# Kernel optimization log

Measured on AMD Instinct MI355X. Metric: run time of the kernel, lower is better.

The kernel has to match this reference:

```python
import jax, jax.numpy as jnp
import numpy as np

N_NODES = 50000
N_EDGES = 600000
D = 128
APPNP_K = 5
APPNP_ALPHA = 0.2


def _mish(x):
    return x * jnp.tanh(jax.nn.softplus(x))


def setup_inputs() -> dict:
    key = jax.random.key(0)
    ks = jax.random.split(key, 6)
    x = jax.random.normal(ks[0], (N_NODES, D), dtype=jnp.float32)
    src = jax.random.randint(ks[1], (N_EDGES,), 0, N_NODES, dtype=jnp.int32)
    dst = jax.random.randint(ks[2], (N_EDGES,), 0, N_NODES, dtype=jnp.int32)
    W1 = jax.random.normal(ks[3], (D, D), dtype=jnp.float32) * (1.0 / np.sqrt(D))
    b1 = jnp.zeros((D,), dtype=jnp.float32)
    W2 = jax.random.normal(ks[4], (2 * D, D), dtype=jnp.float32) * (1.0 / np.sqrt(2 * D))
    b2 = jnp.zeros((D,), dtype=jnp.float32)
    eps1 = jnp.zeros((1,), dtype=jnp.float32)
    eps2 = jnp.zeros((1,), dtype=jnp.float32)
    return {"x": x, "src": src, "dst": dst, "W1": W1, "b1": b1,
            "W2": W2, "b2": b2, "eps1": eps1, "eps2": eps2}


def _appnp(x0, src, dst):
    # DGL APPNPConv: symmetric degree normalization, k power-iteration steps.
    ones = jnp.ones((src.shape[0],), dtype=x0.dtype)
    deg_out = jnp.clip(jax.ops.segment_sum(ones, src, num_segments=N_NODES), 1.0)
    deg_in = jnp.clip(jax.ops.segment_sum(ones, dst, num_segments=N_NODES), 1.0)
    norm_o = deg_out[:, None] ** -0.5  # [N,1]
    norm_i = deg_in[:, None] ** -0.5
    h = x0
    for _ in range(APPNP_K):
        h = h * norm_o
        h = jax.ops.segment_sum(h[src], dst, num_segments=N_NODES)  # gather-scatter
        h = h * norm_i
        h = (1.0 - APPNP_ALPHA) * h + APPNP_ALPHA * x0
    return h


def _gin(h, src, dst, eps, W, b):
    # GINConv(sum, learn_eps): (1+eps)*h + sum_{j in N(i)} h_j, then Linear.
    agg = jax.ops.segment_sum(h[src], dst, num_segments=N_NODES)
    return ((1.0 + eps) * h + agg) @ W + b


def reference(x, src, dst, W1, b1, W2, b2, eps1, eps2):
    out = jnp.tanh(x)           # GCNNorm affects edge weights only; node feats then tanh
    x0 = out                    # res_out[0]
    out = _appnp(out, src, dst)
    out = _gin(out, src, dst, eps1[0], W1, b1)          # layer 0
    out = jnp.concatenate([out, x0], axis=1)            # residual concat
    out = _gin(out, src, dst, eps2[0], W2, b2)          # layer 1
    return _mish(out)
```

## Files before the change

### kernel.cpp

```cpp
#include <hip/hip_runtime.h>
#include <hip/hip_fp16.h>
#include <math.h>

#define NN 50000
#define NE 600000
#define NT ((NN + 31) / 32)

#define HB 64
#define NBIN2 25000

typedef _Float16 half8_t __attribute__((ext_vector_type(8)));
typedef float f32x16 __attribute__((ext_vector_type(16)));
typedef float f32x2 __attribute__((ext_vector_type(2)));

union F2H { float2 f; __half2 h[2]; };

__device__ __forceinline__ float2 fp8_dec(unsigned short u) {
  f32x2 v = __builtin_amdgcn_cvt_pk_f32_fp8((unsigned int)u, false);
  float2 r; r.x = v.x; r.y = v.y; return r;
}
__device__ __forceinline__ unsigned short fp8_enc(float a, float b) {
  return (unsigned short)__builtin_amdgcn_cvt_pk_fp8_f32(a, b, 0u, false);
}


__global__ __launch_bounds__(256) void k_tanh(const float* __restrict__ x,
                                              const float* __restrict__ no,
                                              __half2* __restrict__ x0h,
                                              unsigned int* __restrict__ x0n8,
                                              unsigned int* __restrict__ x0p8) {
  int i = blockIdx.x * 256 + threadIdx.x;
  if (i >= NN * 32) return;
  float4 v = reinterpret_cast<const float4*>(x)[i];
  float t[4];
  float vv[4] = {v.x, v.y, v.z, v.w};
  #pragma unroll
  for (int j = 0; j < 4; ++j) {
    float xc = fminf(fmaxf(vv[j], -9.f), 9.f);
    float E = __expf(2.f * xc);
    t[j] = (E - 1.f) / (E + 1.f);
  }
  float s = no[i >> 5];
  F2H a;
  a.h[0] = __floats2half2_rn(t[0], t[1]);
  a.h[1] = __floats2half2_rn(t[2], t[3]);
  reinterpret_cast<float2*>(x0h)[i] = a.f;
  unsigned int p = __builtin_amdgcn_cvt_pk_fp8_f32(t[0] * s, t[1] * s, 0u, false);
  p = __builtin_amdgcn_cvt_pk_fp8_f32(t[2] * s, t[3] * s, p, true);
  x0n8[i] = p;
  unsigned int q = __builtin_amdgcn_cvt_pk_fp8_f32(t[0], t[1], 0u, false);
  q = __builtin_amdgcn_cvt_pk_fp8_f32(t[2], t[3], q, true);
  x0p8[i] = q;
}

__global__ __launch_bounds__(256) void k_wt(const float* __restrict__ W1,
                                            const float* __restrict__ W2,
                                            _Float16* __restrict__ w1p,
                                            _Float16* __restrict__ w2p) {
  int i = blockIdx.x * 256 + threadIdx.x;
  if (i < 128 * 128) {
    int k = i >> 7, n = i & 127;
    int nb = n >> 5, r = n & 31, ks = k >> 4, g = (k & 15) >> 3, j = k & 7;
    w1p[(((ks << 2) + nb) * 64 + (g << 5) + r) * 8 + j] = (_Float16)W1[i];
  } else {
    int q = i - 128 * 128;
    if (q < 256 * 128) {
      int k = q >> 7, n = q & 127;
      int nb = n >> 5, r = n & 31, ks = k >> 4, g = (k & 15) >> 3, j = k & 7;
      w2p[(((ks << 2) + nb) * 64 + (g << 5) + r) * 8 + j] = (_Float16)W2[q];
    }
  }
}

__global__ __launch_bounds__(1024) void k_hist2(const int* __restrict__ src,
                                                const int* __restrict__ dst,
                                                unsigned int* __restrict__ hpart,
                                                int* __restrict__ lseq) {
  __shared__ unsigned int lh[NBIN2];
  #pragma unroll 1
  for (int ph = 0; ph < 2; ++ph) {
    const int* idx = ph ? dst : src;
    for (int i = threadIdx.x; i < NBIN2; i += 1024) lh[i] = 0;
    __syncthreads();
    if (ph) {
      for (int e = blockIdx.x * 1024 + threadIdx.x; e < NE; e += HB * 1024) {
        int v = idx[e];
        int hi = (v >= NBIN2) ? 1 : 0;
        int bin = v - hi * NBIN2;
        unsigned int old = atomicAdd(&lh[bin], hi ? 65536u : 1u);
        lseq[e] = (int)((old >> (hi * 16)) & 0xffffu);
      }
    } else {
      for (int e = blockIdx.x * 1024 + threadIdx.x; e < NE; e += HB * 1024) {
        int v = idx[e];
        int hi = (v >= NBIN2) ? 1 : 0;
        atomicAdd(&lh[v - hi * NBIN2], hi ? 65536u : 1u);
      }
    }
    __syncthreads();
    unsigned int* outp = hpart + ((size_t)ph * HB + blockIdx.x) * NBIN2;
    for (int i = threadIdx.x; i < NBIN2; i += 1024) outp[i] = lh[i];
    __syncthreads();
  }
}

__global__ __launch_bounds__(256) void k_merge2(unsigned int* __restrict__ hpart,
                                                int* __restrict__ ci,
                                                float* __restrict__ no,
                                                float* __restrict__ ni) {
  int bin = blockIdx.x * 256 + threadIdx.x;
  if (bin >= NBIN2) return;
  const unsigned int* ps = hpart + bin;
  unsigned int* pd = hpart + (size_t)HB * NBIN2 + bin;
  unsigned int so0 = 0, so1 = 0, si0 = 0, si1 = 0;
  #pragma unroll 8
  for (int b = 0; b < HB; ++b) {
    unsigned int v = ps[(size_t)b * NBIN2];
    so0 += v & 0xffffu; so1 += v >> 16;
  }
  #pragma unroll 8
  for (int b = 0; b < HB; ++b) {
    unsigned int* p = pd + (size_t)b * NBIN2;
    unsigned int v = *p;
    *p = si0 | (si1 << 16);
    si0 += v & 0xffffu; si1 += v >> 16;
  }
  ci[bin] = (int)si0;
  ci[bin + NBIN2] = (int)si1;
  no[bin] = rsqrtf((float)max((int)so0, 1));
  no[bin + NBIN2] = rsqrtf((float)max((int)so1, 1));
  ni[bin] = rsqrtf((float)max((int)si0, 1));
  ni[bin + NBIN2] = rsqrtf((float)max((int)si1, 1));
}

__global__ __launch_bounds__(1024) void k_scanA(const int* __restrict__ deg,
                                                int* __restrict__ incl,
                                                int* __restrict__ bsum) {
  int tid = threadIdx.x;
  int gid = blockIdx.x * 1024 + tid;
  int v = (gid < NN) ? deg[gid] : 0;
  int lane = tid & 63;
  #pragma unroll
  for (int o = 1; o < 64; o <<= 1) {
    int n = __shfl_up(v, o);
    if (lane >= o) v += n;
  }
  __shared__ int ws[16];
  int wid = tid >> 6;
  if (lane == 63) ws[wid] = v;
  __syncthreads();
  if (tid < 16) {
    int s = ws[tid];
    #pragma unroll
    for (int o = 1; o < 16; o <<= 1) {
      int n = __shfl_up(s, o);
      if (tid >= o) s += n;
    }
    ws[tid] = s;
  }
  __syncthreads();
  if (wid > 0) v += ws[wid - 1];
  if (gid < NN) incl[gid] = v;
  if (tid == 1023) bsum[blockIdx.x] = v;
}

__global__ __launch_bounds__(64) void k_scanB(const int* __restrict__ bsum,
                                              int* __restrict__ boff, int nb) {
  int t = threadIdx.x;
  int v = (t < nb) ? bsum[t] : 0;
  int orig = v;
  #pragma unroll
  for (int o = 1; o < 64; o <<= 1) {
    int n = __shfl_up(v, o);
    if (t >= o) v += n;
  }
  if (t < nb) boff[t] = v - orig;
}

__global__ __launch_bounds__(256) void k_scanC(const int* __restrict__ incl,
                                               const int* __restrict__ deg,
                                               const int* __restrict__ boff,
                                               int* __restrict__ rp) {
  int i = blockIdx.x * 256 + threadIdx.x;
  if (i < NN) rp[i] = incl[i] - deg[i] + boff[i >> 10];
  if (i == 0) rp[NN] = NE;
}

__global__ __launch_bounds__(256) void k_scatter(const int* __restrict__ src,
                                                 const int* __restrict__ dst,
                                                 const int* __restrict__ lseq,
                                                 const unsigned int* __restrict__ hpart,
                                                 const int* __restrict__ rp,
                                                 int* __restrict__ colsrc) {
  int e = blockIdx.x * 256 + threadIdx.x;
  if (e >= NE) return;
  int d = dst[e];
  int hi = (d >= NBIN2) ? 1 : 0;
  int bin = d - hi * NBIN2;
  int b = (e >> 10) & (HB - 1);
  unsigned int w = hpart[((size_t)HB + b) * NBIN2 + bin];
  int ofs = (int)((w >> (hi * 16)) & 0xffffu);
  colsrc[rp[d] + ofs + lseq[e]] = src[e];
}

#define GATHER_LOOP(LOADEXPR)                                        \
  for (int base = 0; base < cnt; base += 64) {                      \
    int e = beg + base + lane;                                      \
    int cv = (e < end) ? cs[e] : 0;                                 \
    int m = cnt - base; if (m > 64) m = 64;                         \
    int j = 0;                                                      \
    for (; j + 8 <= m; j += 8) {                                    \
      _Pragma("unroll")                                             \
      for (int u = 0; u < 8; ++u) {                                 \
        int s = __builtin_amdgcn_readlane(cv, j + u);               \
        LOADEXPR;                                                   \
      }                                                             \
    }                                                               \
    if (j + 4 <= m) {                                               \
      _Pragma("unroll")                                             \
      for (int u = 0; u < 4; ++u) {                                 \
        int s = __builtin_amdgcn_readlane(cv, j + u);               \
        LOADEXPR;                                                   \
      }                                                             \
      j += 4;                                                       \
    }                                                               \
    if (j + 2 <= m) {                                               \
      _Pragma("unroll")                                             \
      for (int u = 0; u < 2; ++u) {                                 \
        int s = __builtin_amdgcn_readlane(cv, j + u);               \
        LOADEXPR;                                                   \
      }                                                             \
      j += 2;                                                       \
    }                                                               \
    if (j < m) {                                                    \
      int s = __builtin_amdgcn_readlane(cv, j);                     \
      LOADEXPR;                                                     \
    }                                                               \
  }

template <bool LAST>
__global__ __launch_bounds__(256) void k_appnp8(const unsigned short* __restrict__ h8,
                                                const __half2* __restrict__ x0,
                                                const float* __restrict__ no,
                                                const float* __restrict__ ni,
                                                const int* __restrict__ rp,
                                                const int* __restrict__ cs,
                                                unsigned short* __restrict__ out8,
                                                __half2* __restrict__ out16) {
  int w = (blockIdx.x * 256 + threadIdx.x) >> 6;
  int lane = threadIdx.x & 63;
  if (w >= NN) return;
  const unsigned short* hl = h8 + lane;
  int beg = rp[w], end = rp[w + 1], cnt = end - beg;
  float ax = 0.f, ay = 0.f;
  GATHER_LOOP({
    float2 f = fp8_dec(hl[s * 64]);
    ax += f.x; ay += f.y;
  })
  float wi = 0.8f * ni[w];
  float2 xv = __half22float2(x0[w * 64 + lane]);
  float rx = wi * ax + 0.2f * xv.x;
  float ry = wi * ay + 0.2f * xv.y;
  if (LAST) {
    out16[w * 64 + lane] = __floats2half2_rn(rx, ry);
  } else {
    float sc = no[w];
    out8[w * 64 + lane] = fp8_enc(rx * sc, ry * sc);
  }
}

__device__ inline void store_packed(_Float16* __restrict__ zp, int w, int lane,
                                    float v0, float v1) {
  int t = w >> 5, r = w & 31;
  int ks = lane >> 3, g = (lane >> 2) & 1, j = (lane & 3) * 2;
  size_t addr = (((size_t)t * 8 + ks) * 64 + g * 32 + r) * 8 + j;
  *reinterpret_cast<__half2*>(zp + addr) = __floats2half2_rn(v0, v1);
}

__global__ __launch_bounds__(256) void k_appnp_first8(const unsigned short* __restrict__ xn8,
                                                      const unsigned short* __restrict__ xp8,
                                                      const __half2* __restrict__ xp,
                                                      const float* __restrict__ epsp,
                                                      const float* __restrict__ no,
                                                      const float* __restrict__ ni,
                                                      const int* __restrict__ rp,
                                                      const int* __restrict__ cs,
                                                      unsigned short* __restrict__ hout8,
                                                      _Float16* __restrict__ zxout) {
  int w = (blockIdx.x * 256 + threadIdx.x) >> 6;
  int lane = threadIdx.x & 63;
  if (w >= NN) return;
  const unsigned short* xnl = xn8 + lane;
  const unsigned short* xpl = xp8 + lane;
  int beg = rp[w], end = rp[w + 1], cnt = end - beg;
  float ax = 0.f, ay = 0.f, bx = 0.f, by = 0.f;
  GATHER_LOOP({
    float2 f = fp8_dec(xnl[s * 64]);
    float2 g2 = fp8_dec(xpl[s * 64]);
    ax += f.x; ay += f.y; bx += g2.x; by += g2.y;
  })
  float2 xv = __half22float2(xp[w * 64 + lane]);
  float wi = 0.8f * ni[w];
  float sc = no[w];
  hout8[w * 64 + lane] = fp8_enc(sc * (wi * ax + 0.2f * xv.x),
                                 sc * (wi * ay + 0.2f * xv.y));
  float e2 = 1.0f + epsp[0];
  store_packed(zxout, w, lane, e2 * xv.x + bx, e2 * xv.y + by);
}

__global__ __launch_bounds__(256) void k_gz_pair(const __half2* __restrict__ h,
                                                 const float* __restrict__ epsp,
                                                 const int* __restrict__ rp,
                                                 const int* __restrict__ cs,
                                                 _Float16* __restrict__ zout,
                                                 int hf) {
  int wp = (blockIdx.x * 256 + threadIdx.x) >> 6;
  if (wp >= NN / 2) return;
  int lane = threadIdx.x & 63;
  int l31 = lane & 31;
  int w = wp * 2 + (lane >> 5);
  const __half2* hl = h + hf * 32 + l31;
  int beg = rp[w], end = rp[w + 1], cnt = end - beg;
  float ax = 0.f, ay = 0.f;
  for (int base = 0;; base += 32) {
    int m = cnt - base;
    if (m > 32) m = 32;
    int mA = __shfl(m, 0), mB = __shfl(m, 32);
    int mmax = mA > mB ? mA : mB;
    if (mmax <= 0) break;
    int cv = (base + l31 < cnt) ? cs[beg + base + l31] : 0;
    int j = 0;
#define PSTEP(U) { int s = __shfl(cv, j + (U), 32);                    \
                   float2 f = __half22float2(hl[(size_t)s * 64]);      \
                   if (j + (U) < m) { ax += f.x; ay += f.y; } }
    for (; j + 8 <= mmax; j += 8) {
      PSTEP(0) PSTEP(1) PSTEP(2) PSTEP(3) PSTEP(4) PSTEP(5) PSTEP(6) PSTEP(7)
    }
    if (j + 4 <= mmax) { PSTEP(0) PSTEP(1) PSTEP(2) PSTEP(3) j += 4; }
    if (j + 2 <= mmax) { PSTEP(0) PSTEP(1) j += 2; }
    if (j < mmax) { PSTEP(0) }
#undef PSTEP
  }
  float e1 = 1.0f + epsp[0];
  float2 hv = __half22float2(h[(size_t)w * 64 + hf * 32 + l31]);
  int k0 = hf * 64 + l31 * 2;
  int t = w >> 5, r = w & 31;
  int ks = k0 >> 4, g = (k0 >> 3) & 1, jj = k0 & 7;
  size_t addr = (((size_t)t * 8 + ks) * 64 + g * 32 + r) * 8 + jj;
  *reinterpret_cast<__half2*>(zout + addr) =
      __floats2half2_rn(e1 * hv.x + ax, e1 * hv.y + ay);
}

template <int KTOT, bool MISH>
__global__ __launch_bounds__(64) void k_mgemm(const _Float16* __restrict__ z0,
                                              const _Float16* __restrict__ z1,
                                              const _Float16* __restrict__ wp,
                                              const float* __restrict__ bias,
                                              float* __restrict__ outf,
                                              __half2* __restrict__ outh) {
  int lane = threadIdx.x;
  int t = blockIdx.x;
  int row0 = t * 32;
  if (row0 >= NN) return;
  int r31 = lane & 31, g = lane >> 5;
  f32x16 acc[4];
  #pragma unroll
  for (int i = 0; i < 4; ++i) acc[i] = (f32x16)(0.0f);
  #pragma unroll 4
  for (int ks = 0; ks < KTOT / 16; ++ks) {
    const _Float16* zp = (KTOT == 256 && ks >= 8) ? z1 : z0;
    int kls = (KTOT == 256) ? (ks & 7) : ks;
    half8_t a = *reinterpret_cast<const half8_t*>(
        zp + (((size_t)t * 8 + kls) * 64 + lane) * 8);
    #pragma unroll
    for (int nb = 0; nb < 4; ++nb) {
      half8_t b = *reinterpret_cast<const half8_t*>(
          wp + (((size_t)ks * 4 + nb) * 64 + lane) * 8);
      acc[nb] = __builtin_amdgcn_mfma_f32_32x32x16_f16(a, b, acc[nb], 0, 0, 0);
    }
  }
  #pragma unroll
  for (int nb = 0; nb < 4; ++nb) {
    float bv = bias[nb * 32 + r31];
    #pragma unroll
    for (int r = 0; r < 16; ++r) {
      int rl = (r & 3) + 8 * (r >> 2) + 4 * g;
      int grow = row0 + rl;
      if (grow < NN) {
        float v = acc[nb][r] + bv;
        if (MISH) {
          float E = __expf(v);
          float q = E * (E + 2.f);
          float mv = v * q / (q + 2.f);
          v = (v > 15.f) ? v : mv;
          outf[(size_t)grow * 128 + nb * 32 + r31] = v;
        } else {
          float u = __shfl_xor(v, 1);
          if (!(lane & 1)) {
            outh[((size_t)grow * 128 + nb * 32 + r31) >> 1] = __floats2half2_rn(v, u);
          }
        }
      }
    }
  }
}

extern "C" void kernel_launch(void* const* d_in, const int* in_sizes, int n_in,
                              void* d_out, int out_size, void* d_ws, size_t ws_size,
                              hipStream_t stream) {
  const float* x = (const float*)d_in[0];
  const int* src = (const int*)d_in[1];
  const int* dst = (const int*)d_in[2];
  const float* W1 = (const float*)d_in[3];
  const float* b1 = (const float*)d_in[4];
  const float* W2 = (const float*)d_in[5];
  const float* b2 = (const float*)d_in[6];
  const float* eps1 = (const float*)d_in[7];
  const float* eps2 = (const float*)d_in[8];
  float* out = (float*)d_out;

  char* ws = (char*)d_ws;
  size_t off = 0;
  auto alloc = [&](size_t bytes) -> void* {
    void* p = ws + off;
    off += (bytes + 255) & ~(size_t)255;
    return p;
  };
  const size_t NDP = (size_t)NT * 4096;
  __half2* x0h = (__half2*)alloc(NDP * 2);
  unsigned short* x0n8 = (unsigned short*)alloc(NDP);
  unsigned short* x0p8 = (unsigned short*)alloc(NDP);
  unsigned short* hA8 = (unsigned short*)alloc(NDP);
  unsigned short* hB8 = (unsigned short*)alloc(NDP);
  __half2* h5 = (__half2*)alloc(NDP * 2);
  __half2* zx = (__half2*)alloc(NDP * 2);
  __half2* z1p = (__half2*)alloc(NDP * 2);
  __half2* g1h = (__half2*)alloc(NDP * 2);
  __half2* zg = (__half2*)alloc(NDP * 2);
  _Float16* w1p = (_Float16*)alloc(128 * 128 * 2);
  _Float16* w2p = (_Float16*)alloc(256 * 128 * 2);
  int* ci = (int*)alloc(NN * 4);
  float* nrm_o = (float*)alloc(NN * 4);
  float* nrm_i = (float*)alloc(NN * 4);
  int* incl = (int*)alloc(NN * 4);
  int* bsum = (int*)alloc(64 * 4);
  int* boff = (int*)alloc(64 * 4);
  int* rp = (int*)alloc((NN + 1) * 4);
  int* lseq = (int*)alloc(NE * 4);
  int* colsrc = (int*)alloc(NE * 4);

  unsigned int* hpart = (unsigned int*)zx;

  k_hist2<<<HB, 1024, 0, stream>>>(src, dst, hpart, lseq);
  k_merge2<<<(NBIN2 + 255) / 256, 256, 0, stream>>>(hpart, ci, nrm_o, nrm_i);

  const int SB = (NN + 1023) / 1024;
  k_scanA<<<SB, 1024, 0, stream>>>(ci, incl, bsum);
  k_scanB<<<1, 64, 0, stream>>>(bsum, boff, SB);
  k_scanC<<<(NN + 255) / 256, 256, 0, stream>>>(incl, ci, boff, rp);
  const int EB = (NE + 255) / 256;
  k_scatter<<<EB, 256, 0, stream>>>(src, dst, lseq, hpart, rp, colsrc);

  k_tanh<<<(NN * 32 + 255) / 256, 256, 0, stream>>>(x, nrm_o, x0h,
                                                    (unsigned int*)x0n8,
                                                    (unsigned int*)x0p8);
  k_wt<<<192, 256, 0, stream>>>(W1, W2, w1p, w2p);

  const int GB = (NN * 64 + 255) / 256;
  const int GP = (NN / 2 * 64 + 255) / 256;
  k_appnp_first8<<<GB, 256, 0, stream>>>(x0n8, x0p8, x0h, eps2, nrm_o, nrm_i,
                                         rp, colsrc, hA8, (_Float16*)zx);
  k_appnp8<false><<<GB, 256, 0, stream>>>(hA8, x0h, nrm_o, nrm_i, rp, colsrc,
                                          hB8, nullptr);
  k_appnp8<false><<<GB, 256, 0, stream>>>(hB8, x0h, nrm_o, nrm_i, rp, colsrc,
                                          hA8, nullptr);
  k_appnp8<false><<<GB, 256, 0, stream>>>(hA8, x0h, nrm_o, nrm_i, rp, colsrc,
                                          hB8, nullptr);
  k_appnp8<true><<<GB, 256, 0, stream>>>(hB8, x0h, nrm_o, nrm_i, rp, colsrc,
                                         nullptr, h5);

  k_gz_pair<<<GP, 256, 0, stream>>>(h5, eps1, rp, colsrc, (_Float16*)z1p, 0);
  k_gz_pair<<<GP, 256, 0, stream>>>(h5, eps1, rp, colsrc, (_Float16*)z1p, 1);

  k_mgemm<128, false><<<NT, 64, 0, stream>>>((const _Float16*)z1p, nullptr, w1p, b1,
                                             nullptr, g1h);
  k_gz_pair<<<GP, 256, 0, stream>>>(g1h, eps2, rp, colsrc, (_Float16*)zg, 0);
  k_gz_pair<<<GP, 256, 0, stream>>>(g1h, eps2, rp, colsrc, (_Float16*)zg, 1);
  k_mgemm<256, true><<<NT, 64, 0, stream>>>((const _Float16*)zg, (const _Float16*)zx,
                                            w2p, b2, out, nullptr);
}
```

Measured before the change: 275.4 us.

## Process node pairs per wave with half-feature split and interleaved block order

Every gather kernel (the APPNP steps and the GIN aggregation) now uses a pair layout: each wavefront handles two nodes, 32 lanes per node, and covers one half of the feature columns. The grid is remapped so that blocks covering both halves of the same node group sit next to each other, which should improve L2 reuse of the column indices and source rows. The two separate half launches of the GIN aggregation become one launch. This removes the per-node 64-lane wave layout in APPNP, but the two nodes in a wave now step to the longer of their two edge counts, and each index list is read twice.

Result: slower. 308.7 us (+12.1%).

```diff
diff --git a/kernel.cpp b/kernel.cpp
--- a/kernel.cpp
+++ b/kernel.cpp
@@ -8,6 +8,7 @@
 
 #define HB 64
 #define NBIN2 25000
+#define GPIN 12504
 
 typedef _Float16 half8_t __attribute__((ext_vector_type(8)));
 typedef float f32x16 __attribute__((ext_vector_type(16)));
@@ -203,150 +204,117 @@
   colsrc[rp[d] + ofs + lseq[e]] = src[e];
 }
 
-#define GATHER_LOOP(LOADEXPR)                                        \
-  for (int base = 0; base < cnt; base += 64) {                      \
-    int e = beg + base + lane;                                      \
-    int cv = (e < end) ? cs[e] : 0;                                 \
-    int m = cnt - base; if (m > 64) m = 64;                         \
-    int j = 0;                                                      \
-    for (; j + 8 <= m; j += 8) {                                    \
-      _Pragma("unroll")                                             \
-      for (int u = 0; u < 8; ++u) {                                 \
-        int s = __builtin_amdgcn_readlane(cv, j + u);               \
-        LOADEXPR;                                                   \
-      }                                                             \
-    }                                                               \
-    if (j + 4 <= m) {                                               \
-      _Pragma("unroll")                                             \
-      for (int u = 0; u < 4; ++u) {                                 \
-        int s = __builtin_amdgcn_readlane(cv, j + u);               \
-        LOADEXPR;                                                   \
-      }                                                             \
-      j += 4;                                                       \
-    }                                                               \
-    if (j + 2 <= m) {                                               \
-      _Pragma("unroll")                                             \
-      for (int u = 0; u < 2; ++u) {                                 \
-        int s = __builtin_amdgcn_readlane(cv, j + u);               \
-        LOADEXPR;                                                   \
-      }                                                             \
-      j += 2;                                                       \
-    }                                                               \
-    if (j < m) {                                                    \
-      int s = __builtin_amdgcn_readlane(cv, j);                     \
-      LOADEXPR;                                                     \
-    }                                                               \
+#define PAIR_HEAD()                                            \
+  int xb = blockIdx.x & 7;                                     \
+  int hf = xb >> 2;                                            \
+  int bwh = (blockIdx.x >> 3) * 4 + (xb & 3);                  \
+  int pair = bwh * 4 + (threadIdx.x >> 6);                     \
+  if (pair >= NN / 2) return;                                  \
+  int lane = threadIdx.x & 63;                                 \
+  int l31 = lane & 31;                                         \
+  int w = pair * 2 + (lane >> 5);
+
+#define PAIR_LOOP(PSTEP)                                       \
+  int beg = rp[w], end = rp[w + 1], cnt = end - beg;           \
+  for (int base = 0;; base += 32) {                            \
+    int m = cnt - base; if (m > 32) m = 32;                    \
+    int mA = __shfl(m, 0), mB = __shfl(m, 32);                 \
+    int mmax = mA > mB ? mA : mB;                              \
+    if (mmax <= 0) break;                                      \
+    int cv = (base + l31 < cnt) ? cs[beg + base + l31] : 0;    \
+    int j = 0;                                                 \
+    for (; j + 8 <= mmax; j += 8) {                            \
+      PSTEP(0) PSTEP(1) PSTEP(2) PSTEP(3)                      \
+      PSTEP(4) PSTEP(5) PSTEP(6) PSTEP(7)                      \
+    }                                                          \
+    if (j + 4 <= mmax) { PSTEP(0) PSTEP(1) PSTEP(2) PSTEP(3) j += 4; } \
+    if (j + 2 <= mmax) { PSTEP(0) PSTEP(1) j += 2; }           \
+    if (j < mmax) { PSTEP(0) }                                 \
   }
 
 template <bool LAST>
-__global__ __launch_bounds__(256) void k_appnp8(const unsigned short* __restrict__ h8,
-                                                const __half2* __restrict__ x0,
-                                                const float* __restrict__ no,
-                                                const float* __restrict__ ni,
-                                                const int* __restrict__ rp,
-                                                const int* __restrict__ cs,
-                                                unsigned short* __restrict__ out8,
-                                                __half2* __restrict__ out16) {
-  int w = (blockIdx.x * 256 + threadIdx.x) >> 6;
-  int lane = threadIdx.x & 63;
-  if (w >= NN) return;
-  const unsigned short* hl = h8 + lane;
-  int beg = rp[w], end = rp[w + 1], cnt = end - beg;
+__global__ __launch_bounds__(256) void k_appnp8p(const unsigned short* __restrict__ h8,
+                                                 const __half2* __restrict__ x0,
+                                                 const float* __restrict__ no,
+                                                 const float* __restrict__ ni,
+                                                 const int* __restrict__ rp,
+                                                 const int* __restrict__ cs,
+                                                 unsigned short* __restrict__ out8,
+                                                 __half2* __restrict__ out16) {
+  PAIR_HEAD()
+  const unsigned short* hl = h8 + hf * 32 + l31;
   float ax = 0.f, ay = 0.f;
-  GATHER_LOOP({
-    float2 f = fp8_dec(hl[s * 64]);
-    ax += f.x; ay += f.y;
-  })
+#define PS8(U) { int s = __shfl(cv, j + (U), 32);                      \
+                 float2 f = fp8_dec(hl[(size_t)s * 64]);               \
+                 if (j + (U) < m) { ax += f.x; ay += f.y; } }
+  PAIR_LOOP(PS8)
+#undef PS8
   float wi = 0.8f * ni[w];
-  float2 xv = __half22float2(x0[w * 64 + lane]);
+  float2 xv = __half22float2(x0[(size_t)w * 64 + hf * 32 + l31]);
   float rx = wi * ax + 0.2f * xv.x;
   float ry = wi * ay + 0.2f * xv.y;
   if (LAST) {
-    out16[w * 64 + lane] = __floats2half2_rn(rx, ry);
+    out16[(size_t)w * 64 + hf * 32 + l31] = __floats2half2_rn(rx, ry);
   } else {
     float sc = no[w];
-    out8[w * 64 + lane] = fp8_enc(rx * sc, ry * sc);
-  }
-}
-
-__device__ inline void store_packed(_Float16* __restrict__ zp, int w, int lane,
-                                    float v0, float v1) {
-  int t = w >> 5, r = w & 31;
-  int ks = lane >> 3, g = (lane >> 2) & 1, j = (lane & 3) * 2;
-  size_t addr = (((size_t)t * 8 + ks) * 64 + g * 32 + r) * 8 + j;
-  *reinterpret_cast<__half2*>(zp + addr) = __floats2half2_rn(v0, v1);
-}
-
-__global__ __launch_bounds__(256) void k_appnp_first8(const unsigned short* __restrict__ xn8,
-                                                      const unsigned short* __restrict__ xp8,
-                                                      const __half2* __restrict__ xp,
-                                                      const float* __restrict__ epsp,
-                                                      const float* __restrict__ no,
-                                                      const float* __restrict__ ni,
-                                                      const int* __restrict__ rp,
-                                                      const int* __restrict__ cs,
-                                                      unsigned short* __restrict__ hout8,
-                                                      _Float16* __restrict__ zxout) {
-  int w = (blockIdx.x * 256 + threadIdx.x) >> 6;
-  int lane = threadIdx.x & 63;
-  if (w >= NN) return;
-  const unsigned short* xnl = xn8 + lane;
-  const unsigned short* xpl = xp8 + lane;
-  int beg = rp[w], end = rp[w + 1], cnt = end - beg;
+    out8[(size_t)w * 64 + hf * 32 + l31] = fp8_enc(rx * sc, ry * sc);
+  }
+}
+
+__global__ __launch_bounds__(256) void k_first8p(const unsigned short* __restrict__ xn8,
+                                                 const unsigned short* __restrict__ xp8,
+                                                 const __half2* __restrict__ xp,
+                                                 const float* __restrict__ epsp,
+                                                 const float* __restrict__ no,
+                                                 const float* __restrict__ ni,
+                                                 const int* __restrict__ rp,
+                                                 const int* __restrict__ cs,
+                                                 unsigned short* __restrict__ hout8,
+                                                 _Float16* __restrict__ zxout) {
+  PAIR_HEAD()
+  const unsigned short* xnl = xn8 + hf * 32 + l31;
+  const unsigned short* xpl = xp8 + hf * 32 + l31;
   float ax = 0.f, ay = 0.f, bx = 0.f, by = 0.f;
-  GATHER_LOOP({
-    float2 f = fp8_dec(xnl[s * 64]);
-    float2 g2 = fp8_dec(xpl[s * 64]);
-    ax += f.x; ay += f.y; bx += g2.x; by += g2.y;
-  })
-  float2 xv = __half22float2(xp[w * 64 + lane]);
+#define PSD(U) { int s = __shfl(cv, j + (U), 32);                      \
+                 float2 f = fp8_dec(xnl[(size_t)s * 64]);              \
+                 float2 g2 = fp8_dec(xpl[(size_t)s * 64]);             \
+                 if (j + (U) < m) { ax += f.x; ay += f.y;              \
+                                    bx += g2.x; by += g2.y; } }
+  PAIR_LOOP(PSD)
+#undef PSD
+  float2 xv = __half22float2(xp[(size_t)w * 64 + hf * 32 + l31]);
   float wi = 0.8f * ni[w];
   float sc = no[w];
-  hout8[w * 64 + lane] = fp8_enc(sc * (wi * ax + 0.2f * xv.x),
-                                 sc * (wi * ay + 0.2f * xv.y));
+  hout8[(size_t)w * 64 + hf * 32 + l31] = fp8_enc(sc * (wi * ax + 0.2f * xv.x),
+                                                  sc * (wi * ay + 0.2f * xv.y));
   float e2 = 1.0f + epsp[0];
-  store_packed(zxout, w, lane, e2 * xv.x + bx, e2 * xv.y + by);
-}
-
-__global__ __launch_bounds__(256) void k_gz_pair(const __half2* __restrict__ h,
-                                                 const float* __restrict__ epsp,
-                                                 const int* __restrict__ rp,
-                                                 const int* __restrict__ cs,
-                                                 _Float16* __restrict__ zout,
-                                                 int hf) {
-  int wp = (blockIdx.x * 256 + threadIdx.x) >> 6;
-  if (wp >= NN / 2) return;
-  int lane = threadIdx.x & 63;
-  int l31 = lane & 31;
-  int w = wp * 2 + (lane >> 5);
+  int k0 = hf * 64 + l31 * 2;
+  int t = w >> 5, r = w & 31;
+  int ks = k0 >> 4, gg = (k0 >> 3) & 1, jj = k0 & 7;
+  size_t addr = (((size_t)t * 8 + ks) * 64 + gg * 32 + r) * 8 + jj;
+  *reinterpret_cast<__half2*>(zxout + addr) =
+      __floats2half2_rn(e2 * xv.x + bx, e2 * xv.y + by);
+}
+
+__global__ __launch_bounds__(256) void k_gz_pairp(const __half2* __restrict__ h,
+                                                  const float* __restrict__ epsp,
+                                                  const int* __restrict__ rp,
+                                                  const int* __restrict__ cs,
+                                                  _Float16* __restrict__ zout) {
+  PAIR_HEAD()
   const __half2* hl = h + hf * 32 + l31;
-  int beg = rp[w], end = rp[w + 1], cnt = end - beg;
   float ax = 0.f, ay = 0.f;
-  for (int base = 0;; base += 32) {
-    int m = cnt - base;
-    if (m > 32) m = 32;
-    int mA = __shfl(m, 0), mB = __shfl(m, 32);
-    int mmax = mA > mB ? mA : mB;
-    if (mmax <= 0) break;
-    int cv = (base + l31 < cnt) ? cs[beg + base + l31] : 0;
-    int j = 0;
-#define PSTEP(U) { int s = __shfl(cv, j + (U), 32);                    \
-                   float2 f = __half22float2(hl[(size_t)s * 64]);      \
-                   if (j + (U) < m) { ax += f.x; ay += f.y; } }
-    for (; j + 8 <= mmax; j += 8) {
-      PSTEP(0) PSTEP(1) PSTEP(2) PSTEP(3) PSTEP(4) PSTEP(5) PSTEP(6) PSTEP(7)
-    }
-    if (j + 4 <= mmax) { PSTEP(0) PSTEP(1) PSTEP(2) PSTEP(3) j += 4; }
-    if (j + 2 <= mmax) { PSTEP(0) PSTEP(1) j += 2; }
-    if (j < mmax) { PSTEP(0) }
-#undef PSTEP
-  }
+#define PSZ(U) { int s = __shfl(cv, j + (U), 32);                      \
+                 float2 f = __half22float2(hl[(size_t)s * 64]);        \
+                 if (j + (U) < m) { ax += f.x; ay += f.y; } }
+  PAIR_LOOP(PSZ)
+#undef PSZ
   float e1 = 1.0f + epsp[0];
   float2 hv = __half22float2(h[(size_t)w * 64 + hf * 32 + l31]);
   int k0 = hf * 64 + l31 * 2;
   int t = w >> 5, r = w & 31;
-  int ks = k0 >> 4, g = (k0 >> 3) & 1, jj = k0 & 7;
-  size_t addr = (((size_t)t * 8 + ks) * 64 + g * 32 + r) * 8 + jj;
+  int ks = k0 >> 4, gg = (k0 >> 3) & 1, jj = k0 & 7;
+  size_t addr = (((size_t)t * 8 + ks) * 64 + gg * 32 + r) * 8 + jj;
   *reinterpret_cast<__half2*>(zout + addr) =
       __floats2half2_rn(e1 * hv.x + ax, e1 * hv.y + ay);
 }
@@ -466,26 +434,22 @@
                                                     (unsigned int*)x0p8);
   k_wt<<<192, 256, 0, stream>>>(W1, W2, w1p, w2p);
 
-  const int GB = (NN * 64 + 255) / 256;
-  const int GP = (NN / 2 * 64 + 255) / 256;
-  k_appnp_first8<<<GB, 256, 0, stream>>>(x0n8, x0p8, x0h, eps2, nrm_o, nrm_i,
-                                         rp, colsrc, hA8, (_Float16*)zx);
-  k_appnp8<false><<<GB, 256, 0, stream>>>(hA8, x0h, nrm_o, nrm_i, rp, colsrc,
-                                          hB8, nullptr);
-  k_appnp8<false><<<GB, 256, 0, stream>>>(hB8, x0h, nrm_o, nrm_i, rp, colsrc,
-                                          hA8, nullptr);
-  k_appnp8<false><<<GB, 256, 0, stream>>>(hA8, x0h, nrm_o, nrm_i, rp, colsrc,
-                                          hB8, nullptr);
-  k_appnp8<true><<<GB, 256, 0, stream>>>(hB8, x0h, nrm_o, nrm_i, rp, colsrc,
-                                         nullptr, h5);
-
-  k_gz_pair<<<GP, 256, 0, stream>>>(h5, eps1, rp, colsrc, (_Float16*)z1p, 0);
-  k_gz_pair<<<GP, 256, 0, stream>>>(h5, eps1, rp, colsrc, (_Float16*)z1p, 1);
+  k_first8p<<<GPIN, 256, 0, stream>>>(x0n8, x0p8, x0h, eps2, nrm_o, nrm_i,
+                                      rp, colsrc, hA8, (_Float16*)zx);
+  k_appnp8p<false><<<GPIN, 256, 0, stream>>>(hA8, x0h, nrm_o, nrm_i, rp, colsrc,
+                                             hB8, nullptr);
+  k_appnp8p<false><<<GPIN, 256, 0, stream>>>(hB8, x0h, nrm_o, nrm_i, rp, colsrc,
+                                             hA8, nullptr);
+  k_appnp8p<false><<<GPIN, 256, 0, stream>>>(hA8, x0h, nrm_o, nrm_i, rp, colsrc,
+                                             hB8, nullptr);
+  k_appnp8p<true><<<GPIN, 256, 0, stream>>>(hB8, x0h, nrm_o, nrm_i, rp, colsrc,
+                                            nullptr, h5);
+
+  k_gz_pairp<<<GPIN, 256, 0, stream>>>(h5, eps1, rp, colsrc, (_Float16*)z1p);
 
   k_mgemm<128, false><<<NT, 64, 0, stream>>>((const _Float16*)z1p, nullptr, w1p, b1,
                                              nullptr, g1h);
-  k_gz_pair<<<GP, 256, 0, stream>>>(g1h, eps2, rp, colsrc, (_Float16*)zg, 0);
-  k_gz_pair<<<GP, 256, 0, stream>>>(g1h, eps2, rp, colsrc, (_Float16*)zg, 1);
+  k_gz_pairp<<<GPIN, 256, 0, stream>>>(g1h, eps2, rp, colsrc, (_Float16*)zg);
   k_mgemm<256, true><<<NT, 64, 0, stream>>>((const _Float16*)zg, (const _Float16*)zx,
                                             w2p, b2, out, nullptr);
 }
```
